# Performance work log

Measured on AMD Instinct MI355X. Metric: run time of the kernel, lower is better.

Reference implementation:

```python
import jax, jax.numpy as jnp
import numpy as np

VOCAB = 32000
EMB = 256
HID = 512
SEQ = 512
SOS = 1  # word2vec key_to_index['<SOS>']; PAD assumed index 0 and never sampled


def setup_inputs() -> dict:
    key = jax.random.key(0)
    ks = jax.random.split(key, 8)
    k_lstm = 1.0 / np.sqrt(HID)
    k_out = 1.0 / np.sqrt(HID)
    return {
        # token ids in [2, VOCAB) so the PAD-skip branch never triggers
        "input_seq": jax.random.randint(ks[0], (1, SEQ), 2, VOCAB, dtype=jnp.int32),
        "h0": jnp.zeros((1, 1, HID), jnp.float32),
        "c0": jnp.zeros((1, 1, HID), jnp.float32),
        "embedding": jax.random.normal(ks[1], (VOCAB, EMB), jnp.float32) * 0.02,
        "W_ih": jax.random.uniform(ks[2], (4 * HID, EMB), jnp.float32, -k_lstm, k_lstm),
        "W_hh": jax.random.uniform(ks[3], (4 * HID, HID), jnp.float32, -k_lstm, k_lstm),
        "b_ih": jax.random.uniform(ks[4], (4 * HID,), jnp.float32, -k_lstm, k_lstm),
        "b_hh": jax.random.uniform(ks[5], (4 * HID,), jnp.float32, -k_lstm, k_lstm),
        "W_out": jax.random.uniform(ks[6], (VOCAB, HID), jnp.float32, -k_out, k_out),
        "b_out": jax.random.uniform(ks[7], (VOCAB,), jnp.float32, -k_out, k_out),
    }


def reference(input_seq, h0, c0, embedding, W_ih, W_hh, b_ih, b_hh, W_out, b_out):
    # tokens actually fed to the LSTM: <SOS> then the full teacher-forced sequence
    tokens = jnp.concatenate([jnp.array([SOS], jnp.int32), input_seq[0]])  # [S+1]
    emb = embedding[tokens]  # [S+1, E]
    bias = b_ih + b_hh

    def cell(carry, x_t):
        h, c = carry  # [H], [H]
        gates = W_ih @ x_t + W_hh @ h + bias  # [4H], torch gate order i,f,g,o
        i, f, g, o = jnp.split(gates, 4)
        i = jax.nn.sigmoid(i)
        f = jax.nn.sigmoid(f)
        g = jnp.tanh(g)
        o = jax.nn.sigmoid(o)
        c_new = f * c + i * g
        h_new = o * jnp.tanh(c_new)
        return (h_new, c_new), h_new

    (hT, cT), hs = jax.lax.scan(cell, (h0[0, 0], c0[0, 0]), emb)  # hs: [S+1, H]
    logits = hs @ W_out.T + b_out  # [S+1, V] (same math as per-step Linear + cat)
    outputs = logits[None]  # [1, S+1, V]
    return outputs, hT[None, None], cT[None, None]
```

## Files before the change

kernel.cpp:

```cpp
#include <hip/hip_runtime.h>
#include <cmath>

#define VOCAB 32000
#define EMB   256
#define HID   512
#define TLEN  513
#define G4    2048
#define NWAVE 128
#define SOS   1

typedef unsigned long long u64;
typedef unsigned int uivec4 __attribute__((ext_vector_type(4)));
typedef float f32x4 __attribute__((ext_vector_type(4)));
typedef short bf16x8 __attribute__((ext_vector_type(8)));

__device__ inline float fsig(float x)  { return __builtin_amdgcn_rcpf(1.f + __expf(-x)); }
__device__ inline float ftanh(float x) { return 1.f - 2.f * __builtin_amdgcn_rcpf(__expf(2.f * x) + 1.f); }
__device__ inline float fma4(f32x4 w, f32x4 h, float a) {
    return fmaf(w[0], h[0], fmaf(w[1], h[1], fmaf(w[2], h[2], fmaf(w[3], h[3], a))));
}

__device__ inline void bf16split(float f, short& h, short& l) {
    unsigned u = __float_as_uint(f);
    unsigned r = u + (0x7fffu + ((u >> 16) & 1u));
    unsigned hb = r & 0xffff0000u;
    h = (short)(hb >> 16);
    float res = f - __uint_as_float(hb);
    unsigned u2 = __float_as_uint(res);
    unsigned r2 = u2 + (0x7fffu + ((u2 >> 16) & 1u));
    l = (short)(r2 >> 16);
}

__global__ __launch_bounds__(256) void precompute_gates(
    const int* __restrict__ seq, const float* __restrict__ emb,
    const float* __restrict__ W_ih, const float* __restrict__ b_ih,
    const float* __restrict__ b_hh, float* __restrict__ Xg, u64* pk)
{
    __shared__ __align__(16) float ebuf[16][EMB];
    const int bt = blockIdx.x;
    const int br = blockIdx.y;
    const int tid = threadIdx.x;

    if (bt == 0 && br == 0) {
        pk[tid] = 0; pk[tid + 256] = 0; pk[tid + 512] = 0; pk[tid + 768] = 0;
    }

    for (int tt = 0; tt < 16; ++tt) {
        int t = bt * 16 + tt;
        if (t < TLEN) {
            int tok = (t == 0) ? SOS : seq[t - 1];
            ebuf[tt][tid] = emb[(size_t)tok * EMB + tid];
        }
    }
    __syncthreads();

    const int row = br * 256 + tid;
    float acc[16];
#pragma unroll
    for (int tt = 0; tt < 16; ++tt) acc[tt] = 0.f;

    const float4* wp = (const float4*)(W_ih + (size_t)row * EMB);
#pragma unroll 4
    for (int k4 = 0; k4 < EMB / 4; ++k4) {
        float4 w = wp[k4];
#pragma unroll
        for (int tt = 0; tt < 16; ++tt) {
            float4 e = *(const float4*)&ebuf[tt][k4 * 4];
            acc[tt] = fmaf(w.x, e.x, fmaf(w.y, e.y, fmaf(w.z, e.z, fmaf(w.w, e.w, acc[tt]))));
        }
    }

    const float bias = b_ih[row] + b_hh[row];
    for (int tt = 0; tt < 16; ++tt) {
        int t = bt * 16 + tt;
        if (t < TLEN) Xg[(size_t)t * G4 + row] = acc[tt] + bias;
    }
}

__global__ __launch_bounds__(64, 1) void lstm_recurrence(
    const float* __restrict__ Xg, const float* __restrict__ W_hh,
    const float* __restrict__ h0, const float* __restrict__ c0,
    float* __restrict__ hs, u64* pk,
    float* __restrict__ out_hT, float* __restrict__ out_cT)
{
    const int W  = blockIdx.x;
    const int ln = threadIdx.x;
    const int qs = (ln >> 2) & 3;
    const int ds = ln & 3;
    const int j4 = 4 * W;

    f32x4 wa[16], wb[16];
#pragma unroll
    for (int r = 0; r < 16; ++r) {
        const float* wp = W_hh + ((size_t)(r >> 2) * HID + j4 + (r & 3)) * HID + 8 * ln;
        wa[r] = *(const f32x4*)wp;
        wb[r] = *(const f32x4*)(wp + 4);
    }
#pragma unroll
    for (int r = 0; r < 16; ++r) {
        asm volatile("" : "+v"(wa[r]), "+v"(wb[r]));
    }

    float c = (ln < 4) ? c0[j4 + ln] : 0.f;

    f32x4 hA, hB;
    {
        const float* hp = h0 + 8 * ln;
        hA = *(const f32x4*)hp;
        hB = *(const f32x4*)(hp + 4);
    }

    for (int t = 0; t < TLEN; ++t) {
        float xg = Xg[(size_t)t * G4 + qs * HID + j4 + ds];

        if (t > 0) {
            const unsigned tt = (unsigned)t;
            u64 sa = (u64)(uintptr_t)(pk + (size_t)(t & 1) * HID + 8 * ln);
            uivec4 r0, r1, r2, r3;
            for (;;) {
                asm volatile(
                    "global_load_dwordx4 %0, %4, off sc0 sc1\n\t"
                    "global_load_dwordx4 %1, %4, off offset:16 sc0 sc1\n\t"
                    "global_load_dwordx4 %2, %4, off offset:32 sc0 sc1\n\t"
                    "global_load_dwordx4 %3, %4, off offset:48 sc0 sc1\n\t"
                    "s_waitcnt vmcnt(0)"
                    : "=&v"(r0), "=&v"(r1), "=&v"(r2), "=&v"(r3) : "v"(sa));
                if (r0.y == tt && r0.w == tt && r1.y == tt && r1.w == tt &&
                    r2.y == tt && r2.w == tt && r3.y == tt && r3.w == tt) break;
            }
            hA[0] = __uint_as_float(r0.x); hA[1] = __uint_as_float(r0.z);
            hA[2] = __uint_as_float(r1.x); hA[3] = __uint_as_float(r1.z);
            hB[0] = __uint_as_float(r2.x); hB[1] = __uint_as_float(r2.z);
            hB[2] = __uint_as_float(r3.x); hB[3] = __uint_as_float(r3.z);
        }

        float p[16];
#pragma unroll
        for (int r = 0; r < 16; ++r)
            p[r] = fma4(wa[r], hA, fma4(wb[r], hB, 0.f));

        const bool b0 = (ln & 1), b1 = (ln & 2), b2 = (ln & 4), b3 = (ln & 8);
        float q1[8];
#pragma unroll
        for (int i = 0; i < 8; ++i) {
            float mine = b0 ? p[2*i+1] : p[2*i];
            float send = b0 ? p[2*i]   : p[2*i+1];
            q1[i] = mine + __shfl_xor(send, 1, 64);
        }
        float q2[4];
#pragma unroll
        for (int i = 0; i < 4; ++i) {
            float mine = b1 ? q1[2*i+1] : q1[2*i];
            float send = b1 ? q1[2*i]   : q1[2*i+1];
            q2[i] = mine + __shfl_xor(send, 2, 64);
        }
        float q3[2];
#pragma unroll
        for (int i = 0; i < 2; ++i) {
            float mine = b2 ? q2[2*i+1] : q2[2*i];
            float send = b2 ? q2[2*i]   : q2[2*i+1];
            q3[i] = mine + __shfl_xor(send, 4, 64);
        }
        float q4;
        {
            float mine = b3 ? q3[1] : q3[0];
            float send = b3 ? q3[0] : q3[1];
            q4 = mine + __shfl_xor(send, 8, 64);
        }
        q4 += __shfl_xor(q4, 16, 64);
        q4 += __shfl_xor(q4, 32, 64);
        float gate = q4 + xg;

        float v = (qs == 2) ? ftanh(gate) : fsig(gate);
        float iv = __shfl(v, ds,      64);
        float fv = __shfl(v, 4 + ds,  64);
        float gv = __shfl(v, 8 + ds,  64);
        float ov = __shfl(v, 12 + ds, 64);
        c = fmaf(fv, c, iv * gv);
        float h_ = ov * ftanh(c);

        if (ln < 4) {
            if (t < TLEN - 1) {
                u64 word = ((u64)(unsigned)(t + 1) << 32) | (u64)__float_as_uint(h_);
                __hip_atomic_store(&pk[(size_t)((t + 1) & 1) * HID + j4 + ln], word,
                                   __ATOMIC_RELAXED, __HIP_MEMORY_SCOPE_AGENT);
            } else {
                out_hT[j4 + ln] = h_;
                out_cT[j4 + ln] = c;
            }
            hs[(size_t)t * HID + j4 + ln] = h_;
        }
    }
}

#define GLDT 40

__global__ __launch_bounds__(256, 2) void out_gemm_mfma(
    const float* __restrict__ hs, const float* __restrict__ W_out,
    const float* __restrict__ b_out, float* __restrict__ out)
{
    __shared__ __align__(16) short Ah[128][GLDT];
    __shared__ __align__(16) short Al[128][GLDT];
    __shared__ __align__(16) short Bh[128][GLDT];
    __shared__ __align__(16) short Bl[128][GLDT];

    const int tb = blockIdx.x;
    const int vb = blockIdx.y;
    const int tid = threadIdx.x;
    const int w   = tid >> 6;
    const int l   = tid & 63;
    const int l15 = l & 15;
    const int lg  = l >> 4;
    const int m0 = tb * 128, n0 = vb * 128;

    const int sr = tid >> 1;
    const int kh = (tid & 1) * 16;

    f32x4 acc[2][8];
#pragma unroll
    for (int s = 0; s < 2; ++s)
#pragma unroll
        for (int cc = 0; cc < 8; ++cc) acc[s][cc] = (f32x4){0.f, 0.f, 0.f, 0.f};

    for (int k0 = 0; k0 < HID; k0 += 32) {
        {
            int trow = m0 + sr;
            float4 fa0 = make_float4(0.f,0.f,0.f,0.f), fa1 = fa0, fa2 = fa0, fa3 = fa0;
            if (trow < TLEN) {
                const float4* ap = (const float4*)(hs + (size_t)trow * HID + k0 + kh);
                fa0 = ap[0]; fa1 = ap[1]; fa2 = ap[2]; fa3 = ap[3];
            }
            float fv[16] = { fa0.x,fa0.y,fa0.z,fa0.w, fa1.x,fa1.y,fa1.z,fa1.w,
                             fa2.x,fa2.y,fa2.z,fa2.w, fa3.x,fa3.y,fa3.z,fa3.w };
#pragma unroll
            for (int g = 0; g < 2; ++g) {
                union { short s[8]; bf16x8 v; } ph, pl;
#pragma unroll
                for (int e = 0; e < 8; ++e) bf16split(fv[g * 8 + e], ph.s[e], pl.s[e]);
                *(bf16x8*)&Ah[sr][kh + 8 * g] = ph.v;
                *(bf16x8*)&Al[sr][kh + 8 * g] = pl.v;
            }
        }
        {
            const float4* bp = (const float4*)(W_out + (size_t)(n0 + sr) * HID + k0 + kh);
            float4 fb0 = bp[0], fb1 = bp[1], fb2 = bp[2], fb3 = bp[3];
            float fv[16] = { fb0.x,fb0.y,fb0.z,fb0.w, fb1.x,fb1.y,fb1.z,fb1.w,
                             fb2.x,fb2.y,fb2.z,fb2.w, fb3.x,fb3.y,fb3.z,fb3.w };
#pragma unroll
            for (int g = 0; g < 2; ++g) {
                union { short s[8]; bf16x8 v; } ph, pl;
#pragma unroll
                for (int e = 0; e < 8; ++e) bf16split(fv[g * 8 + e], ph.s[e], pl.s[e]);
                *(bf16x8*)&Bh[sr][kh + 8 * g] = ph.v;
                *(bf16x8*)&Bl[sr][kh + 8 * g] = pl.v;
            }
        }
        __syncthreads();

        bf16x8 ah[2], al2[2];
#pragma unroll
        for (int s = 0; s < 2; ++s) {
            ah[s]  = *(const bf16x8*)&Ah[32 * w + 16 * s + l15][8 * lg];
            al2[s] = *(const bf16x8*)&Al[32 * w + 16 * s + l15][8 * lg];
        }
#pragma unroll
        for (int cc = 0; cc < 8; ++cc) {
            bf16x8 bh = *(const bf16x8*)&Bh[16 * cc + l15][8 * lg];
            bf16x8 bl = *(const bf16x8*)&Bl[16 * cc + l15][8 * lg];
#pragma unroll
            for (int s = 0; s < 2; ++s) {
                acc[s][cc] = __builtin_amdgcn_mfma_f32_16x16x32_bf16(ah[s],  bh, acc[s][cc], 0, 0, 0);
                acc[s][cc] = __builtin_amdgcn_mfma_f32_16x16x32_bf16(ah[s],  bl, acc[s][cc], 0, 0, 0);
                acc[s][cc] = __builtin_amdgcn_mfma_f32_16x16x32_bf16(al2[s], bh, acc[s][cc], 0, 0, 0);
            }
        }
        __syncthreads();
    }

#pragma unroll
    for (int cc = 0; cc < 8; ++cc) {
        int col = n0 + 16 * cc + l15;
        float bo = b_out[col];
#pragma unroll
        for (int s = 0; s < 2; ++s) {
            int rbase = m0 + 32 * w + 16 * s + lg * 4;
#pragma unroll
            for (int r = 0; r < 4; ++r) {
                int trow = rbase + r;
                if (trow < TLEN) out[(size_t)trow * VOCAB + col] = acc[s][cc][r] + bo;
            }
        }
    }
}

extern "C" void kernel_launch(void* const* d_in, const int* in_sizes, int n_in,
                              void* d_out, int out_size, void* d_ws, size_t ws_size,
                              hipStream_t stream)
{
    const int*   seq   = (const int*)  d_in[0];
    const float* h0    = (const float*)d_in[1];
    const float* c0    = (const float*)d_in[2];
    const float* emb   = (const float*)d_in[3];
    const float* W_ih  = (const float*)d_in[4];
    const float* W_hh  = (const float*)d_in[5];
    const float* b_ih  = (const float*)d_in[6];
    const float* b_hh  = (const float*)d_in[7];
    const float* W_out = (const float*)d_in[8];
    const float* b_out = (const float*)d_in[9];

    float* out_logits = (float*)d_out;
    float* out_hT     = out_logits + (size_t)TLEN * VOCAB;
    float* out_cT     = out_hT + HID;

    float* Xg = (float*)d_ws;
    float* hs = Xg + (size_t)TLEN * G4;
    u64*   pk = (u64*)(hs + (size_t)TLEN * HID);

    precompute_gates<<<dim3(33, 8), 256, 0, stream>>>(seq, emb, W_ih, b_ih, b_hh, Xg, pk);
    lstm_recurrence<<<NWAVE, 64, 0, stream>>>(Xg, W_hh, h0, c0, hs, pk, out_hT, out_cT);
    out_gemm_mfma<<<dim3(5, 250), 256, 0, stream>>>(hs, W_out, b_out, out_logits);
}
```

Before: 993.6 us.

## Fuse input-gate precompute into recurrence kernel with per-block LDS gate buffer

Removes the separate precompute_gates kernel. Each recurrence block now computes the input projections for its own 16 gate rows across all timesteps using 256 threads and keeps them in LDS, then drops to one wave for the recurrence. This avoids writing and re-reading the Xg buffer in global memory and saves one kernel launch, replacing them with a memset for the flag buffer. The cost is that each block redundantly gathers the embedding rows, and the prologue runs before the serial recurrence, which sits on the critical path.

```diff
diff --git a/kernel.cpp b/kernel.cpp
--- a/kernel.cpp
+++ b/kernel.cpp
@@ -6,7 +6,7 @@
 #define HID   512
 #define TLEN  513
 #define G4    2048
-#define NWAVE 128
+#define NBLK  128
 #define SOS   1
 
 typedef unsigned long long u64;
@@ -31,63 +31,45 @@
     l = (short)(r2 >> 16);
 }
 
-__global__ __launch_bounds__(256) void precompute_gates(
+__global__ __launch_bounds__(256, 1) void rec_fused(
     const int* __restrict__ seq, const float* __restrict__ emb,
     const float* __restrict__ W_ih, const float* __restrict__ b_ih,
-    const float* __restrict__ b_hh, float* __restrict__ Xg, u64* pk)
-{
-    __shared__ __align__(16) float ebuf[16][EMB];
-    const int bt = blockIdx.x;
-    const int br = blockIdx.y;
-    const int tid = threadIdx.x;
-
-    if (bt == 0 && br == 0) {
-        pk[tid] = 0; pk[tid + 256] = 0; pk[tid + 512] = 0; pk[tid + 768] = 0;
-    }
-
-    for (int tt = 0; tt < 16; ++tt) {
-        int t = bt * 16 + tt;
-        if (t < TLEN) {
-            int tok = (t == 0) ? SOS : seq[t - 1];
-            ebuf[tt][tid] = emb[(size_t)tok * EMB + tid];
-        }
-    }
-    __syncthreads();
-
-    const int row = br * 256 + tid;
-    float acc[16];
-#pragma unroll
-    for (int tt = 0; tt < 16; ++tt) acc[tt] = 0.f;
-
-    const float4* wp = (const float4*)(W_ih + (size_t)row * EMB);
-#pragma unroll 4
-    for (int k4 = 0; k4 < EMB / 4; ++k4) {
-        float4 w = wp[k4];
-#pragma unroll
-        for (int tt = 0; tt < 16; ++tt) {
-            float4 e = *(const float4*)&ebuf[tt][k4 * 4];
-            acc[tt] = fmaf(w.x, e.x, fmaf(w.y, e.y, fmaf(w.z, e.z, fmaf(w.w, e.w, acc[tt]))));
-        }
-    }
-
-    const float bias = b_ih[row] + b_hh[row];
-    for (int tt = 0; tt < 16; ++tt) {
-        int t = bt * 16 + tt;
-        if (t < TLEN) Xg[(size_t)t * G4 + row] = acc[tt] + bias;
-    }
-}
-
-__global__ __launch_bounds__(64, 1) void lstm_recurrence(
-    const float* __restrict__ Xg, const float* __restrict__ W_hh,
+    const float* __restrict__ b_hh, const float* __restrict__ W_hh,
     const float* __restrict__ h0, const float* __restrict__ c0,
     float* __restrict__ hs, u64* pk,
     float* __restrict__ out_hT, float* __restrict__ out_cT)
 {
-    const int W  = blockIdx.x;
-    const int ln = threadIdx.x;
+    __shared__ __align__(16) float xg_lds[TLEN * 16];
+
+    const int W   = blockIdx.x;
+    const int tid = threadIdx.x;
+    const int j4  = 4 * W;
+
+    {
+        const int r  = tid & 15;
+        const int grow = (r >> 2) * HID + j4 + (r & 3);
+        const float bias = b_ih[grow] + b_hh[grow];
+        const f32x4* wp = (const f32x4*)(W_ih + (size_t)grow * EMB);
+        for (int t = (tid >> 4); t < TLEN; t += 16) {
+            int tok = (t == 0) ? SOS : seq[t - 1];
+            const f32x4* ep = (const f32x4*)(emb + (size_t)tok * EMB);
+            float a0 = 0.f, a1 = 0.f, a2 = 0.f, a3 = 0.f;
+#pragma unroll 4
+            for (int k = 0; k < EMB / 16; ++k) {
+                a0 = fma4(wp[4 * k],     ep[4 * k],     a0);
+                a1 = fma4(wp[4 * k + 1], ep[4 * k + 1], a1);
+                a2 = fma4(wp[4 * k + 2], ep[4 * k + 2], a2);
+                a3 = fma4(wp[4 * k + 3], ep[4 * k + 3], a3);
+            }
+            xg_lds[t * 16 + r] = ((a0 + a1) + (a2 + a3)) + bias;
+        }
+    }
+    __syncthreads();
+    if (tid >= 64) return;
+
+    const int ln = tid;
     const int qs = (ln >> 2) & 3;
     const int ds = ln & 3;
-    const int j4 = 4 * W;
 
     f32x4 wa[16], wb[16];
 #pragma unroll
@@ -111,7 +93,7 @@
     }
 
     for (int t = 0; t < TLEN; ++t) {
-        float xg = Xg[(size_t)t * G4 + qs * HID + j4 + ds];
+        float xg = xg_lds[t * 16 + (ln & 15)];
 
         if (t > 0) {
             const unsigned tt = (unsigned)t;
@@ -312,11 +294,11 @@
     float* out_hT     = out_logits + (size_t)TLEN * VOCAB;
     float* out_cT     = out_hT + HID;
 
-    float* Xg = (float*)d_ws;
-    float* hs = Xg + (size_t)TLEN * G4;
+    float* hs = (float*)d_ws;
     u64*   pk = (u64*)(hs + (size_t)TLEN * HID);
 
-    precompute_gates<<<dim3(33, 8), 256, 0, stream>>>(seq, emb, W_ih, b_ih, b_hh, Xg, pk);
-    lstm_recurrence<<<NWAVE, 64, 0, stream>>>(Xg, W_hh, h0, c0, hs, pk, out_hT, out_cT);
+    hipMemsetAsync(pk, 0, 2 * HID * sizeof(u64), stream);
+    rec_fused<<<NBLK, 256, 0, stream>>>(seq, emb, W_ih, b_ih, b_hh, W_hh,
+                                        h0, c0, hs, pk, out_hT, out_cT);
     out_gemm_mfma<<<dim3(5, 250), 256, 0, stream>>>(hs, W_out, b_out, out_logits);
 }
```

Result: slower. 1.390 ms (+39.8%).
